# Optimization experiments

Measured on AMD Instinct MI355X. Metric: run time of the kernel, lower is better.

Reference implementation:

```python
import jax, jax.numpy as jnp
import numpy as np

K = 10
ALPHA = 0.1

def setup_inputs() -> dict:
    key = jax.random.key(0)
    k1, k2, k3, k4 = jax.random.split(key, 4)
    N, E, IN, HID, OUT = 100000, 3200000, 512, 256, 64
    x = jax.random.normal(k1, (N, IN), dtype=jnp.float32)
    edge_index = jax.random.randint(k2, (2, E), 0, N, dtype=jnp.int64)
    W1 = jax.random.normal(k3, (IN, HID), dtype=jnp.float32) * (1.0 / np.sqrt(IN))
    b1 = jnp.zeros((HID,), jnp.float32)
    W2 = jax.random.normal(k4, (HID, OUT), dtype=jnp.float32) * (1.0 / np.sqrt(HID))
    b2 = jnp.zeros((OUT,), jnp.float32)
    return {"x": x, "edge_index": edge_index, "W1": W1, "b1": b1, "W2": W2, "b2": b2}

def reference(x, edge_index, W1, b1, W2, b2):
    N = x.shape[0]
    # gcn_norm with self-loops (PyG default for APPNP)
    loop = jnp.arange(N, dtype=edge_index.dtype)
    src = jnp.concatenate([edge_index[0], loop])  # [E+N]
    dst = jnp.concatenate([edge_index[1], loop])
    ones = jnp.ones(src.shape[0], dtype=x.dtype)
    deg = jax.ops.segment_sum(ones, dst, num_segments=N)
    dis = jnp.where(deg > 0, jax.lax.rsqrt(deg), 0.0)
    norm = dis[src] * dis[dst]  # [E+N]

    # 2-layer MLP (dropout disabled: eval mode)
    h = jnp.maximum(x @ W1 + b1, 0.0) @ W2 + b2  # [N, out]

    # K-step PPR diffusion: z <- alpha*h + (1-alpha)*A_hat z
    def step(z, _):
        agg = jax.ops.segment_sum(norm[:, None] * z[src], dst, num_segments=N)
        return ALPHA * h + (1.0 - ALPHA) * agg, None

    z, _ = jax.lax.scan(step, h, None, length=K)
    return jax.nn.log_softmax(z, axis=-1)
```

## Files before the change

### kernel.cpp

```cpp
#include <hip/hip_runtime.h>
#include <hip/hip_bf16.h>

#define ALPHA_F 0.1f
#define KSTEPS 10
#define BKT_SH 9
#define P1_CHUNK 8192

typedef __attribute__((ext_vector_type(8))) short bf16x8;
typedef __attribute__((ext_vector_type(4))) float f32x4;

__device__ __forceinline__ unsigned short f2bf(float f) {
  union { float f; unsigned int u; } v; v.f = f;
  unsigned int u = v.u;
  u += 0x7FFFu + ((u >> 16) & 1u);
  return (unsigned short)(u >> 16);
}
__device__ __forceinline__ float bflo(unsigned int u) { return __uint_as_float(u << 16); }
__device__ __forceinline__ float bfhi(unsigned int u) { return __uint_as_float(u & 0xFFFF0000u); }

__device__ __forceinline__ void gload16(const void* g, void* l) {
  __builtin_amdgcn_global_load_lds(
      (const __attribute__((address_space(1))) void*)g,
      (__attribute__((address_space(3))) void*)l, 16, 0, 0);
}


__global__ __launch_bounds__(256)
void p0_hist(const int* __restrict__ dstv, int E, int* __restrict__ bhist) {
  __shared__ int h[256];
  int t = threadIdx.x;
  h[t] = 0;
  __syncthreads();
  int b0 = blockIdx.x * P1_CHUNK;
  int lim = min(P1_CHUNK, E - b0);
  for (int i = t; i < lim; i += 256) atomicAdd(&h[dstv[b0 + i] >> BKT_SH], 1);
  __syncthreads();
  if (h[t]) atomicAdd(&bhist[t], h[t]);
}

__global__ void p0_scan(const int* __restrict__ bhist, int* __restrict__ bbase,
                        int* __restrict__ gcur, int* __restrict__ rowptr, int N, int E) {
  __shared__ int s[256];
  int t = threadIdx.x;
  int mine = bhist[t];
  s[t] = mine;
  __syncthreads();
  for (int off = 1; off < 256; off <<= 1) {
    int v = (t >= off) ? s[t - off] : 0;
    __syncthreads();
    s[t] += v;
    __syncthreads();
  }
  int excl = s[t] - mine;
  bbase[t] = excl;
  gcur[t] = excl;
  if (t == 0) rowptr[N] = E;
}

__global__ __launch_bounds__(256)
void p1_scatter(const int* __restrict__ srcv, const int* __restrict__ dstv, int E,
                int* __restrict__ gcur, int2* __restrict__ tmp) {
  __shared__ int h[256];
  __shared__ int loc[256];
  int t = threadIdx.x;
  int b0 = blockIdx.x * P1_CHUNK;
  int lim = min(P1_CHUNK, E - b0);
  h[t] = 0;
  __syncthreads();
  for (int i = t; i < lim; i += 256) atomicAdd(&h[dstv[b0 + i] >> BKT_SH], 1);
  __syncthreads();
  loc[t] = h[t] ? atomicAdd(&gcur[t], h[t]) : 0;
  __syncthreads();
  h[t] = 0;
  __syncthreads();
  for (int i = t; i < lim; i += 256) {
    int d = dstv[b0 + i], s = srcv[b0 + i];
    int b = d >> BKT_SH;
    int pos = loc[b] + atomicAdd(&h[b], 1);
    tmp[pos] = make_int2(s, d);
  }
}

__global__ __launch_bounds__(256)
void p2_bucket(const int2* __restrict__ tmp, const int* __restrict__ bbase,
               const int* __restrict__ bhist, int* __restrict__ counts,
               int* __restrict__ rowptr, int2* __restrict__ out, int N) {
  __shared__ int h1[512];
  __shared__ int cur[512];
  __shared__ int s2[256];
  const int t = threadIdx.x;
  const int b = blockIdx.x;
  const int base = bbase[b];
  const int sz = bhist[b];
  const int r0 = b << BKT_SH;
  const int nrows = min(512, N - r0);

  h1[t] = 0; h1[t + 256] = 0;
  __syncthreads();
  for (int i = t; i < sz; i += 256) atomicAdd(&h1[tmp[base + i].y - r0], 1);
  __syncthreads();
  if (t < nrows) counts[r0 + t] = h1[t];
  if (t + 256 < nrows) counts[r0 + t + 256] = h1[t + 256];
  int a = h1[2 * t], c = h1[2 * t + 1];
  s2[t] = a + c;
  __syncthreads();
  for (int off = 1; off < 256; off <<= 1) {
    int v = (t >= off) ? s2[t - off] : 0;
    __syncthreads();
    s2[t] += v;
    __syncthreads();
  }
  int excl2 = s2[t] - (a + c);
  cur[2 * t] = excl2;
  cur[2 * t + 1] = excl2 + a;
  __syncthreads();
  if (t < nrows) rowptr[r0 + t] = base + cur[t];
  if (t + 256 < nrows) rowptr[r0 + t + 256] = base + cur[t + 256];
  __syncthreads();
  for (int i = t; i < sz; i += 256) {
    int2 e = tmp[base + i];
    int p = base + atomicAdd(&cur[e.y - r0], 1);
    out[p] = e;
  }
}

__global__ void k_dis(const int* __restrict__ counts, float* __restrict__ dis, int N) {
  int i = blockIdx.x * 256 + threadIdx.x;
  if (i < N) dis[i] = rsqrtf((float)(counts[i] + 1));
}

__global__ void p3_weights(int2* __restrict__ edges, const float* __restrict__ dis, int E) {
  int i = blockIdx.x * 256 + threadIdx.x;
  if (i >= E) return;
  int2 e = edges[i];
  edges[i] = make_int2(e.x, __float_as_int(dis[e.x] * dis[e.y]));
}


__global__ void k_wconv1(const float* __restrict__ W, unsigned short* __restrict__ WT) {
  int idx = blockIdx.x * 256 + threadIdx.x;
  if (idx >= 512 * 256) return;
  int e = idx & 7, n = (idx >> 3) & 15, q = (idx >> 7) & 7;
  int nsub = (idx >> 10) & 15, kstep = idx >> 14;
  int k = kstep * 64 + q * 8 + e;
  int ncol = nsub * 16 + n;
  WT[idx] = f2bf(W[(size_t)k * 256 + ncol]);
}

__global__ void k_wconv2(const float* __restrict__ W, unsigned short* __restrict__ WT) {
  int idx = blockIdx.x * 256 + threadIdx.x;
  if (idx >= 256 * 64) return;
  int e = idx & 7, n = (idx >> 3) & 15, q = (idx >> 7) & 7;
  int nsub = (idx >> 10) & 3, kstep = idx >> 12;
  int k = kstep * 64 + q * 8 + e;
  int ncol = nsub * 16 + n;
  WT[idx] = f2bf(W[(size_t)k * 64 + ncol]);
}

__global__ __launch_bounds__(512)
void gemm1_kernel(const float* __restrict__ X, const unsigned short* __restrict__ Bt,
                  const float* __restrict__ bias, unsigned short* __restrict__ outT,
                  int M) {
  __shared__ __align__(16) unsigned short Al[8192];
  __shared__ __align__(16) unsigned short Bl[16384];
  const int t = threadIdx.x;
  const int m0 = blockIdx.x * 128;
  const int lane = t & 63;
  const int w = t >> 6;
  const int wm = w >> 2, wn = w & 3;

  const int sm = ((t >> 7) << 4) + (t & 15);
  const int sq = (t >> 4) & 7;
  const int r1 = m0 + sm;
  const int r2 = r1 + 64;
  const bool g1 = r1 < M, g2 = r2 < M;

  f32x4 acc[4][4] = {};

  for (int ks = 0; ks < 8; ++ks) {
    const int kc = ks * 64 + sq * 8;
    uint4 v1 = {0, 0, 0, 0}, v2 = {0, 0, 0, 0};
    if (g1) {
      const float* p = X + (size_t)r1 * 512 + kc;
      float4 a = *(const float4*)p, b = *(const float4*)(p + 4);
      unsigned short* o = (unsigned short*)&v1;
      o[0] = f2bf(a.x); o[1] = f2bf(a.y); o[2] = f2bf(a.z); o[3] = f2bf(a.w);
      o[4] = f2bf(b.x); o[5] = f2bf(b.y); o[6] = f2bf(b.z); o[7] = f2bf(b.w);
    }
    if (g2) {
      const float* p = X + (size_t)r2 * 512 + kc;
      float4 a = *(const float4*)p, b = *(const float4*)(p + 4);
      unsigned short* o = (unsigned short*)&v2;
      o[0] = f2bf(a.x); o[1] = f2bf(a.y); o[2] = f2bf(a.z); o[3] = f2bf(a.w);
      o[4] = f2bf(b.x); o[5] = f2bf(b.y); o[6] = f2bf(b.z); o[7] = f2bf(b.w);
    }
    *(uint4*)&Al[t * 8] = v1;
    *(uint4*)&Al[(t + 512) * 8] = v2;

    const unsigned short* bs = Bt + ks * 16384;
    gload16(bs + (size_t)t * 8,          &Bl[t * 8]);
    gload16(bs + (size_t)(t + 512) * 8,  &Bl[(t + 512) * 8]);
    gload16(bs + (size_t)(t + 1024) * 8, &Bl[(t + 1024) * 8]);
    gload16(bs + (size_t)(t + 1536) * 8, &Bl[(t + 1536) * 8]);
    __syncthreads();

#pragma unroll
    for (int kk = 0; kk < 2; ++kk) {
      bf16x8 af[4], bfv[4];
#pragma unroll
      for (int mi = 0; mi < 4; ++mi)
        af[mi] = *(const bf16x8*)&Al[((wm * 4 + mi) * 128 + kk * 64 + (lane >> 4) * 16 + (lane & 15)) * 8];
#pragma unroll
      for (int ni = 0; ni < 4; ++ni)
        bfv[ni] = *(const bf16x8*)&Bl[((wn * 4 + ni) * 128 + kk * 64 + (lane >> 4) * 16 + (lane & 15)) * 8];
#pragma unroll
      for (int mi = 0; mi < 4; ++mi)
#pragma unroll
        for (int ni = 0; ni < 4; ++ni)
          acc[mi][ni] = __builtin_amdgcn_mfma_f32_16x16x32_bf16(af[mi], bfv[ni], acc[mi][ni], 0, 0, 0);
    }
    __syncthreads();
  }

  unsigned short* ob = outT + (size_t)blockIdx.x * 32768;
#pragma unroll
  for (int mi = 0; mi < 4; ++mi) {
#pragma unroll
    for (int ni = 0; ni < 4; ++ni) {
      int n = wn * 64 + ni * 16 + (lane & 15);
      float bv = bias[n];
      int kstep = n >> 6, q = (n >> 3) & 7, e = n & 7;
#pragma unroll
      for (int j = 0; j < 4; ++j) {
        int lm = wm * 64 + mi * 16 + (lane >> 4) * 4 + j;
        if (m0 + lm < M) {
          float v = fmaxf(acc[mi][ni][j] + bv, 0.f);
          int msub = lm >> 4, mm = lm & 15;
          ob[((((kstep * 8 + msub) * 8 + q) * 16 + mm) * 8) + e] = f2bf(v);
        }
      }
    }
  }
}

__global__ __launch_bounds__(256)
void gemm2_kernel(const unsigned short* __restrict__ At, const unsigned short* __restrict__ Bt,
                  const float* __restrict__ bias, unsigned short* __restrict__ hb, int M) {
  __shared__ __align__(16) unsigned short Al[8192];
  __shared__ __align__(16) unsigned short Bl[4096];
  const int t = threadIdx.x;
  const int m0 = blockIdx.x * 128;
  const int lane = t & 63;
  const int w = t >> 6;
  const int wm = w >> 1, wn = w & 1;

  f32x4 acc[4][2] = {};

  const unsigned short* ab = At + (size_t)blockIdx.x * 32768;
  for (int ks = 0; ks < 4; ++ks) {
    const unsigned short* as = ab + ks * 8192;
    gload16(as + (size_t)t * 8,         &Al[t * 8]);
    gload16(as + (size_t)(t + 256) * 8, &Al[(t + 256) * 8]);
    gload16(as + (size_t)(t + 512) * 8, &Al[(t + 512) * 8]);
    gload16(as + (size_t)(t + 768) * 8, &Al[(t + 768) * 8]);
    const unsigned short* bs = Bt + ks * 4096;
    gload16(bs + (size_t)t * 8,         &Bl[t * 8]);
    gload16(bs + (size_t)(t + 256) * 8, &Bl[(t + 256) * 8]);
    __syncthreads();

#pragma unroll
    for (int kk = 0; kk < 2; ++kk) {
      bf16x8 af[4], bfv[2];
#pragma unroll
      for (int mi = 0; mi < 4; ++mi)
        af[mi] = *(const bf16x8*)&Al[((wm * 4 + mi) * 128 + kk * 64 + (lane >> 4) * 16 + (lane & 15)) * 8];
#pragma unroll
      for (int ni = 0; ni < 2; ++ni)
        bfv[ni] = *(const bf16x8*)&Bl[((wn * 2 + ni) * 128 + kk * 64 + (lane >> 4) * 16 + (lane & 15)) * 8];
#pragma unroll
      for (int mi = 0; mi < 4; ++mi)
#pragma unroll
        for (int ni = 0; ni < 2; ++ni)
          acc[mi][ni] = __builtin_amdgcn_mfma_f32_16x16x32_bf16(af[mi], bfv[ni], acc[mi][ni], 0, 0, 0);
    }
    __syncthreads();
  }

#pragma unroll
  for (int mi = 0; mi < 4; ++mi) {
#pragma unroll
    for (int ni = 0; ni < 2; ++ni) {
      int gn = wn * 32 + ni * 16 + (lane & 15);
      float bv = bias[gn];
#pragma unroll
      for (int j = 0; j < 4; ++j) {
        int gm = m0 + wm * 64 + mi * 16 + (lane >> 4) * 4 + j;
        if (gm < M) hb[(size_t)gm * 64 + gn] = f2bf(acc[mi][ni][j] + bv);
      }
    }
  }
}

template<bool FINAL>
__global__ __launch_bounds__(256)
void prop_kernel(const unsigned short* __restrict__ zin,
                 const unsigned short* __restrict__ hb,
                 void* __restrict__ zout, const int* __restrict__ rowptr,
                 const int2* __restrict__ edges, const float* __restrict__ dis, int N) {
  int wid = (blockIdx.x * 256 + threadIdx.x) >> 6;
  wid = __builtin_amdgcn_readfirstlane(wid);
  if (wid >= N) return;
  const int lane = threadIdx.x & 63;
  const int g  = lane >> 3;
  const int lg = lane & 7;
  const int r = wid;

  float acc[8] = {0.f, 0.f, 0.f, 0.f, 0.f, 0.f, 0.f, 0.f};
  const int start = rowptr[r], end = rowptr[r + 1];
  for (int e = start; e < end; e += 64) {
    int na = end - e; if (na > 64) na = 64;
    int2 ed = make_int2(0, 0);
    if (lane < na) ed = edges[e + lane];
#pragma unroll 4
    for (int j = 0; j < na; j += 8) {
      int jj = j + g;
      int cj = __shfl(ed.x, jj);
      float wj = __shfl(__int_as_float(ed.y), jj);
      uint4 zr = *(const uint4*)(zin + (size_t)cj * 64 + 8 * lg);
      acc[0] += wj * bflo(zr.x); acc[1] += wj * bfhi(zr.x);
      acc[2] += wj * bflo(zr.y); acc[3] += wj * bfhi(zr.y);
      acc[4] += wj * bflo(zr.z); acc[5] += wj * bfhi(zr.z);
      acc[6] += wj * bflo(zr.w); acc[7] += wj * bfhi(zr.w);
    }
  }
#pragma unroll
  for (int k = 0; k < 8; ++k) {
    acc[k] += __shfl_xor(acc[k], 8);
    acc[k] += __shfl_xor(acc[k], 16);
    acc[k] += __shfl_xor(acc[k], 32);
  }

  float dr = dis[r];
  float sw = dr * dr;
  uint4 zs = *(const uint4*)(zin + (size_t)r * 64 + 8 * lg);
  uint4 hr = *(const uint4*)(hb + (size_t)r * 64 + 8 * lg);
  float selfz[8] = { bflo(zs.x), bfhi(zs.x), bflo(zs.y), bfhi(zs.y),
                     bflo(zs.z), bfhi(zs.z), bflo(zs.w), bfhi(zs.w) };
  float hv[8]    = { bflo(hr.x), bfhi(hr.x), bflo(hr.y), bfhi(hr.y),
                     bflo(hr.z), bfhi(hr.z), bflo(hr.w), bfhi(hr.w) };
  float f[8];
#pragma unroll
  for (int k = 0; k < 8; ++k)
    f[k] = ALPHA_F * hv[k] + (1.f - ALPHA_F) * (acc[k] + sw * selfz[k]);

  if (!FINAL) {
    if (g == 0) {
      uint4 o;
      o.x = (unsigned)f2bf(f[0]) | ((unsigned)f2bf(f[1]) << 16);
      o.y = (unsigned)f2bf(f[2]) | ((unsigned)f2bf(f[3]) << 16);
      o.z = (unsigned)f2bf(f[4]) | ((unsigned)f2bf(f[5]) << 16);
      o.w = (unsigned)f2bf(f[6]) | ((unsigned)f2bf(f[7]) << 16);
      *(uint4*)((unsigned short*)zout + (size_t)r * 64 + 8 * lg) = o;
    }
  } else {
    float m = f[0];
#pragma unroll
    for (int k = 1; k < 8; ++k) m = fmaxf(m, f[k]);
    m = fmaxf(m, __shfl_xor(m, 1));
    m = fmaxf(m, __shfl_xor(m, 2));
    m = fmaxf(m, __shfl_xor(m, 4));
    float s = 0.f;
#pragma unroll
    for (int k = 0; k < 8; ++k) s += __expf(f[k] - m);
    s += __shfl_xor(s, 1);
    s += __shfl_xor(s, 2);
    s += __shfl_xor(s, 4);
    float ls = __logf(s);
    if (g == 0) {
      float* op = (float*)zout + (size_t)r * 64 + 8 * lg;
      *(float4*)op       = make_float4(f[0] - m - ls, f[1] - m - ls, f[2] - m - ls, f[3] - m - ls);
      *(float4*)(op + 4) = make_float4(f[4] - m - ls, f[5] - m - ls, f[6] - m - ls, f[7] - m - ls);
    }
  }
}

extern "C" void kernel_launch(void* const* d_in, const int* in_sizes, int n_in,
                              void* d_out, int out_size, void* d_ws, size_t ws_size,
                              hipStream_t stream) {
  const float* x  = (const float*)d_in[0];
  const int*   ei = (const int*)d_in[1];
  const float* W1 = (const float*)d_in[2];
  const float* b1 = (const float*)d_in[3];
  const float* W2 = (const float*)d_in[4];
  const float* b2 = (const float*)d_in[5];

  const int IN = 512, HID = 256, OUT = 64;
  const int N = in_sizes[0] / IN;
  const int E = in_sizes[1] / 2;
  const int* srcv = ei;
  const int* dstv = ei + E;
  const int NBUCK = (N + (1 << BKT_SH) - 1) >> BKT_SH;
  const int MT = (N + 127) / 128;

  char* p = (char*)d_ws;
  auto alloc = [&](size_t bytes) -> void* {
    void* r = (void*)p;
    p += (bytes + 255) & ~(size_t)255;
    return r;
  };
  int*   bhist  = (int*)alloc(256 * 4);
  int*   bbase  = (int*)alloc(256 * 4);
  int*   gcur   = (int*)alloc(256 * 4);
  int*   counts = (int*)alloc((size_t)N * 4);
  float* dis    = (float*)alloc((size_t)N * 4);
  int*   rowptr = (int*)alloc((size_t)(N + 1) * 4);
  int2*  edges  = (int2*)alloc((size_t)E * 8);
  unsigned short* WT1t = (unsigned short*)alloc((size_t)IN * HID * 2);
  unsigned short* WT2t = (unsigned short*)alloc((size_t)HID * OUT * 2);
  unsigned short* hidT = (unsigned short*)alloc((size_t)MT * 32768 * 2);
  unsigned short* hb   = (unsigned short*)alloc((size_t)N * OUT * 2);
  int2* tmp = (int2*)hidT;
  unsigned short* zA = hidT;
  unsigned short* zB = hidT + (size_t)N * OUT;

  hipMemsetAsync(bhist, 0, 256 * 4, stream);

  const int p1blocks = (E + P1_CHUNK - 1) / P1_CHUNK;
  p0_hist<<<p1blocks, 256, 0, stream>>>(dstv, E, bhist);
  p0_scan<<<1, 256, 0, stream>>>(bhist, bbase, gcur, rowptr, N, E);
  p1_scatter<<<p1blocks, 256, 0, stream>>>(srcv, dstv, E, gcur, tmp);
  p2_bucket<<<NBUCK, 256, 0, stream>>>(tmp, bbase, bhist, counts, rowptr, edges, N);
  k_dis<<<(N + 255) / 256, 256, 0, stream>>>(counts, dis, N);
  p3_weights<<<(E + 255) / 256, 256, 0, stream>>>(edges, dis, E);

  k_wconv1<<<(IN * HID + 255) / 256, 256, 0, stream>>>(W1, WT1t);
  k_wconv2<<<(HID * OUT + 255) / 256, 256, 0, stream>>>(W2, WT2t);

  gemm1_kernel<<<MT, 512, 0, stream>>>(x, WT1t, b1, hidT, N);
  gemm2_kernel<<<MT, 256, 0, stream>>>(hidT, WT2t, b2, hb, N);

  const int pblocks = (N + 3) / 4;
  const unsigned short* zcur = hb;
  for (int it = 0; it < KSTEPS - 1; ++it) {
    unsigned short* znext = (it & 1) ? zB : zA;
    prop_kernel<false><<<pblocks, 256, 0, stream>>>(zcur, hb, znext, rowptr, edges, dis, N);
    zcur = znext;
  }
  prop_kernel<true><<<pblocks, 256, 0, stream>>>(zcur, hb, d_out, rowptr, edges, dis, N);
}
```

Measured before the change: 820.2 us.

## Split features into per-XCD quarter planes and fold norm into prescaled features

```diff
diff --git a/kernel.cpp b/kernel.cpp
--- a/kernel.cpp
+++ b/kernel.cpp
@@ -84,7 +84,7 @@
 __global__ __launch_bounds__(256)
 void p2_bucket(const int2* __restrict__ tmp, const int* __restrict__ bbase,
                const int* __restrict__ bhist, int* __restrict__ counts,
-               int* __restrict__ rowptr, int2* __restrict__ out, int N) {
+               int* __restrict__ rowptr, int* __restrict__ col, int N) {
   __shared__ int h1[512];
   __shared__ int cur[512];
   __shared__ int s2[256];
@@ -120,7 +120,7 @@
   for (int i = t; i < sz; i += 256) {
     int2 e = tmp[base + i];
     int p = base + atomicAdd(&cur[e.y - r0], 1);
-    out[p] = e;
+    col[p] = e.x;
   }
 }
 
@@ -129,13 +129,12 @@
   if (i < N) dis[i] = rsqrtf((float)(counts[i] + 1));
 }
 
-__global__ void p3_weights(int2* __restrict__ edges, const float* __restrict__ dis, int E) {
-  int i = blockIdx.x * 256 + threadIdx.x;
-  if (i >= E) return;
-  int2 e = edges[i];
-  edges[i] = make_int2(e.x, __float_as_int(dis[e.x] * dis[e.y]));
-}
-
+__global__ void k_zrow(unsigned short* __restrict__ yA, unsigned short* __restrict__ yB, int N) {
+  int t = threadIdx.x;
+  size_t N1 = (size_t)N + 1;
+  if (t < 64)      yA[((size_t)(t >> 4) * N1 + N) * 16 + (t & 15)] = 0;
+  else { int u = t - 64; yB[((size_t)(u >> 4) * N1 + N) * 16 + (u & 15)] = 0; }
+}
 
 __global__ void k_wconv1(const float* __restrict__ W, unsigned short* __restrict__ WT) {
   int idx = blockIdx.x * 256 + threadIdx.x;
@@ -245,7 +244,8 @@
 
 __global__ __launch_bounds__(256)
 void gemm2_kernel(const unsigned short* __restrict__ At, const unsigned short* __restrict__ Bt,
-                  const float* __restrict__ bias, unsigned short* __restrict__ hb, int M) {
+                  const float* __restrict__ bias, const float* __restrict__ dis,
+                  unsigned short* __restrict__ hq, unsigned short* __restrict__ y0, int M) {
   __shared__ __align__(16) unsigned short Al[8192];
   __shared__ __align__(16) unsigned short Bl[4096];
   const int t = threadIdx.x;
@@ -253,6 +253,7 @@
   const int lane = t & 63;
   const int w = t >> 6;
   const int wm = w >> 1, wn = w & 1;
+  const size_t N1 = (size_t)M + 1;
 
   f32x4 acc[4][2] = {};
 
@@ -292,10 +293,15 @@
     for (int ni = 0; ni < 2; ++ni) {
       int gn = wn * 32 + ni * 16 + (lane & 15);
       float bv = bias[gn];
+      int qq = gn >> 4, cc = gn & 15;
 #pragma unroll
       for (int j = 0; j < 4; ++j) {
         int gm = m0 + wm * 64 + mi * 16 + (lane >> 4) * 4 + j;
-        if (gm < M) hb[(size_t)gm * 64 + gn] = f2bf(acc[mi][ni][j] + bv);
+        if (gm < M) {
+          float v = acc[mi][ni][j] + bv;
+          hq[((size_t)qq * M + gm) * 16 + cc] = f2bf(v);
+          y0[((size_t)qq * N1 + gm) * 16 + cc] = f2bf(dis[gm] * v);
+        }
       }
     }
   }
@@ -303,85 +309,71 @@
 
 template<bool FINAL>
 __global__ __launch_bounds__(256)
-void prop_kernel(const unsigned short* __restrict__ zin,
-                 const unsigned short* __restrict__ hb,
-                 void* __restrict__ zout, const int* __restrict__ rowptr,
-                 const int2* __restrict__ edges, const float* __restrict__ dis, int N) {
-  int wid = (blockIdx.x * 256 + threadIdx.x) >> 6;
-  wid = __builtin_amdgcn_readfirstlane(wid);
-  if (wid >= N) return;
+void prop_q(const unsigned short* __restrict__ yin, const unsigned short* __restrict__ hq,
+            void* __restrict__ yout, const int* __restrict__ rowptr,
+            const int* __restrict__ col, const float* __restrict__ dis, int N, int Q) {
+  const int x = blockIdx.x;
+  const int xcd = x & 7;
+  const int q = xcd >> 1;
+  const int i = (x >> 3) * 2 + (xcd & 1);
+  if (i >= Q) return;
+  int r = i * 4 + (threadIdx.x >> 6);
+  if (r >= N) return;
+  r = __builtin_amdgcn_readfirstlane(r);
   const int lane = threadIdx.x & 63;
-  const int g  = lane >> 3;
-  const int lg = lane & 7;
-  const int r = wid;
-
-  float acc[8] = {0.f, 0.f, 0.f, 0.f, 0.f, 0.f, 0.f, 0.f};
+  const int g = lane >> 3;
+  const int lc = lane & 7;
+  const size_t N1 = (size_t)N + 1;
+  const unsigned short* yq = yin + (size_t)q * N1 * 16;
+
+  float a0 = 0.f, a1 = 0.f;
   const int start = rowptr[r], end = rowptr[r + 1];
   for (int e = start; e < end; e += 64) {
     int na = end - e; if (na > 64) na = 64;
-    int2 ed = make_int2(0, 0);
-    if (lane < na) ed = edges[e + lane];
+    int c = N;
+    if (lane < na) c = col[e + lane];
 #pragma unroll 4
     for (int j = 0; j < na; j += 8) {
-      int jj = j + g;
-      int cj = __shfl(ed.x, jj);
-      float wj = __shfl(__int_as_float(ed.y), jj);
-      uint4 zr = *(const uint4*)(zin + (size_t)cj * 64 + 8 * lg);
-      acc[0] += wj * bflo(zr.x); acc[1] += wj * bfhi(zr.x);
-      acc[2] += wj * bflo(zr.y); acc[3] += wj * bfhi(zr.y);
-      acc[4] += wj * bflo(zr.z); acc[5] += wj * bfhi(zr.z);
-      acc[6] += wj * bflo(zr.w); acc[7] += wj * bfhi(zr.w);
-    }
-  }
-#pragma unroll
-  for (int k = 0; k < 8; ++k) {
-    acc[k] += __shfl_xor(acc[k], 8);
-    acc[k] += __shfl_xor(acc[k], 16);
-    acc[k] += __shfl_xor(acc[k], 32);
-  }
+      int cj = __shfl(c, j + g);
+      unsigned v = *(const unsigned*)(yq + (size_t)cj * 16 + 2 * lc);
+      a0 += bflo(v); a1 += bfhi(v);
+    }
+  }
+  a0 += __shfl_xor(a0, 8);  a1 += __shfl_xor(a1, 8);
+  a0 += __shfl_xor(a0, 16); a1 += __shfl_xor(a1, 16);
+  a0 += __shfl_xor(a0, 32); a1 += __shfl_xor(a1, 32);
 
   float dr = dis[r];
-  float sw = dr * dr;
-  uint4 zs = *(const uint4*)(zin + (size_t)r * 64 + 8 * lg);
-  uint4 hr = *(const uint4*)(hb + (size_t)r * 64 + 8 * lg);
-  float selfz[8] = { bflo(zs.x), bfhi(zs.x), bflo(zs.y), bfhi(zs.y),
-                     bflo(zs.z), bfhi(zs.z), bflo(zs.w), bfhi(zs.w) };
-  float hv[8]    = { bflo(hr.x), bfhi(hr.x), bflo(hr.y), bfhi(hr.y),
-                     bflo(hr.z), bfhi(hr.z), bflo(hr.w), bfhi(hr.w) };
-  float f[8];
-#pragma unroll
-  for (int k = 0; k < 8; ++k)
-    f[k] = ALPHA_F * hv[k] + (1.f - ALPHA_F) * (acc[k] + sw * selfz[k]);
-
+  unsigned sv = *(const unsigned*)(yq + (size_t)r * 16 + 2 * lc);
+  unsigned hv = *(const unsigned*)(hq + ((size_t)q * N + r) * 16 + 2 * lc);
+  float f0 = ALPHA_F * bflo(hv) + (1.f - ALPHA_F) * dr * (a0 + bflo(sv));
+  float f1 = ALPHA_F * bfhi(hv) + (1.f - ALPHA_F) * dr * (a1 + bfhi(sv));
   if (!FINAL) {
     if (g == 0) {
-      uint4 o;
-      o.x = (unsigned)f2bf(f[0]) | ((unsigned)f2bf(f[1]) << 16);
-      o.y = (unsigned)f2bf(f[2]) | ((unsigned)f2bf(f[3]) << 16);
-      o.z = (unsigned)f2bf(f[4]) | ((unsigned)f2bf(f[5]) << 16);
-      o.w = (unsigned)f2bf(f[6]) | ((unsigned)f2bf(f[7]) << 16);
-      *(uint4*)((unsigned short*)zout + (size_t)r * 64 + 8 * lg) = o;
+      unsigned o = (unsigned)f2bf(dr * f0) | ((unsigned)f2bf(dr * f1) << 16);
+      *(unsigned*)((unsigned short*)yout + ((size_t)q * N1 + r) * 16 + 2 * lc) = o;
     }
   } else {
-    float m = f[0];
-#pragma unroll
-    for (int k = 1; k < 8; ++k) m = fmaxf(m, f[k]);
-    m = fmaxf(m, __shfl_xor(m, 1));
-    m = fmaxf(m, __shfl_xor(m, 2));
-    m = fmaxf(m, __shfl_xor(m, 4));
-    float s = 0.f;
-#pragma unroll
-    for (int k = 0; k < 8; ++k) s += __expf(f[k] - m);
-    s += __shfl_xor(s, 1);
-    s += __shfl_xor(s, 2);
-    s += __shfl_xor(s, 4);
-    float ls = __logf(s);
     if (g == 0) {
-      float* op = (float*)zout + (size_t)r * 64 + 8 * lg;
-      *(float4*)op       = make_float4(f[0] - m - ls, f[1] - m - ls, f[2] - m - ls, f[3] - m - ls);
-      *(float4*)(op + 4) = make_float4(f[4] - m - ls, f[5] - m - ls, f[6] - m - ls, f[7] - m - ls);
-    }
-  }
+      *(float2*)((float*)yout + ((size_t)q * N + r) * 16 + 2 * lc) = make_float2(f0, f1);
+    }
+  }
+}
+
+__global__ __launch_bounds__(256)
+void k_lsm(const float* __restrict__ zfin, float* __restrict__ out, int N) {
+  int r = (blockIdx.x * 256 + threadIdx.x) >> 6;
+  if (r >= N) return;
+  int lane = threadIdx.x & 63;
+  float v = zfin[((size_t)(lane >> 4) * N + r) * 16 + (lane & 15)];
+  float m = v;
+#pragma unroll
+  for (int off = 32; off; off >>= 1) m = fmaxf(m, __shfl_xor(m, off));
+  float e = __expf(v - m);
+  float s = e;
+#pragma unroll
+  for (int off = 32; off; off >>= 1) s += __shfl_xor(s, off);
+  out[(size_t)r * 64 + lane] = v - m - __logf(s);
 }
 
 extern "C" void kernel_launch(void* const* d_in, const int* in_sizes, int n_in,
@@ -401,6 +393,7 @@
   const int* dstv = ei + E;
   const int NBUCK = (N + (1 << BKT_SH) - 1) >> BKT_SH;
   const int MT = (N + 127) / 128;
+  const size_t N1 = (size_t)N + 1;
 
   char* p = (char*)d_ws;
   auto alloc = [&](size_t bytes) -> void* {
@@ -414,14 +407,22 @@
   int*   counts = (int*)alloc((size_t)N * 4);
   float* dis    = (float*)alloc((size_t)N * 4);
   int*   rowptr = (int*)alloc((size_t)(N + 1) * 4);
-  int2*  edges  = (int2*)alloc((size_t)E * 8);
+  int*   col    = (int*)alloc((size_t)E * 4);
   unsigned short* WT1t = (unsigned short*)alloc((size_t)IN * HID * 2);
   unsigned short* WT2t = (unsigned short*)alloc((size_t)HID * OUT * 2);
-  unsigned short* hidT = (unsigned short*)alloc((size_t)MT * 32768 * 2);
-  unsigned short* hb   = (unsigned short*)alloc((size_t)N * OUT * 2);
-  int2* tmp = (int2*)hidT;
-  unsigned short* zA = hidT;
-  unsigned short* zB = hidT + (size_t)N * OUT;
+  unsigned short* hq   = (unsigned short*)alloc((size_t)N * 64 * 2);
+  unsigned short* yA   = (unsigned short*)alloc(N1 * 64 * 2);
+  size_t hidT_bytes = (size_t)MT * 32768 * 2;
+  size_t zfin_bytes = (size_t)N * 64 * 4;
+  size_t yB_bytes   = N1 * 64 * 2;
+  size_t R_bytes = hidT_bytes;
+  if ((size_t)E * 8 > R_bytes) R_bytes = (size_t)E * 8;
+  if (zfin_bytes + 256 + yB_bytes > R_bytes) R_bytes = zfin_bytes + 256 + yB_bytes;
+  char* R = (char*)alloc(R_bytes);
+  int2* tmp = (int2*)R;
+  unsigned short* hidT = (unsigned short*)R;
+  float* zfin = (float*)R;
+  unsigned short* yB = (unsigned short*)(R + ((zfin_bytes + 255) & ~(size_t)255));
 
   hipMemsetAsync(bhist, 0, 256 * 4, stream);
 
@@ -429,22 +430,24 @@
   p0_hist<<<p1blocks, 256, 0, stream>>>(dstv, E, bhist);
   p0_scan<<<1, 256, 0, stream>>>(bhist, bbase, gcur, rowptr, N, E);
   p1_scatter<<<p1blocks, 256, 0, stream>>>(srcv, dstv, E, gcur, tmp);
-  p2_bucket<<<NBUCK, 256, 0, stream>>>(tmp, bbase, bhist, counts, rowptr, edges, N);
+  p2_bucket<<<NBUCK, 256, 0, stream>>>(tmp, bbase, bhist, counts, rowptr, col, N);
   k_dis<<<(N + 255) / 256, 256, 0, stream>>>(counts, dis, N);
-  p3_weights<<<(E + 255) / 256, 256, 0, stream>>>(edges, dis, E);
 
   k_wconv1<<<(IN * HID + 255) / 256, 256, 0, stream>>>(W1, WT1t);
   k_wconv2<<<(HID * OUT + 255) / 256, 256, 0, stream>>>(W2, WT2t);
 
   gemm1_kernel<<<MT, 512, 0, stream>>>(x, WT1t, b1, hidT, N);
-  gemm2_kernel<<<MT, 256, 0, stream>>>(hidT, WT2t, b2, hb, N);
-
-  const int pblocks = (N + 3) / 4;
-  const unsigned short* zcur = hb;
+  gemm2_kernel<<<MT, 256, 0, stream>>>(hidT, WT2t, b2, dis, hq, yA, N);
+  k_zrow<<<1, 128, 0, stream>>>(yA, yB, N);
+
+  const int Q = (N + 3) / 4;
+  const int pblocks = 8 * ((Q + 1) / 2);
+  const unsigned short* ycur = yA;
   for (int it = 0; it < KSTEPS - 1; ++it) {
-    unsigned short* znext = (it & 1) ? zB : zA;
-    prop_kernel<false><<<pblocks, 256, 0, stream>>>(zcur, hb, znext, rowptr, edges, dis, N);
-    zcur = znext;
-  }
-  prop_kernel<true><<<pblocks, 256, 0, stream>>>(zcur, hb, d_out, rowptr, edges, dis, N);
-}
+    unsigned short* ynext = (it & 1) ? yA : yB;
+    prop_q<false><<<pblocks, 256, 0, stream>>>(ycur, hq, ynext, rowptr, col, dis, N, Q);
+    ycur = ynext;
+  }
+  prop_q<true><<<pblocks, 256, 0, stream>>>(ycur, hq, zfin, rowptr, col, dis, N, Q);
+  k_lsm<<<(N + 3) / 4, 256, 0, stream>>>(zfin, (float*)d_out, N);
+}
```

Result: slower. 1.571 ms (+91.6%).

## Prescale features by inverse-sqrt degree and use padded index-only CSR

Applied to the files above, without the earlier changes.

```diff
diff --git a/kernel.cpp b/kernel.cpp
--- a/kernel.cpp
+++ b/kernel.cpp
@@ -5,6 +5,7 @@
 #define KSTEPS 10
 #define BKT_SH 9
 #define P1_CHUNK 8192
+#define MAXPAD_PER_BUCKET (512 * 32)
 
 typedef __attribute__((ext_vector_type(8))) short bf16x8;
 typedef __attribute__((ext_vector_type(4))) float f32x4;
@@ -39,7 +40,7 @@
 }
 
 __global__ void p0_scan(const int* __restrict__ bhist, int* __restrict__ bbase,
-                        int* __restrict__ gcur, int* __restrict__ rowptr, int N, int E) {
+                        int* __restrict__ gcur) {
   __shared__ int s[256];
   int t = threadIdx.x;
   int mine = bhist[t];
@@ -54,7 +55,6 @@
   int excl = s[t] - mine;
   bbase[t] = excl;
   gcur[t] = excl;
-  if (t == 0) rowptr[N] = E;
 }
 
 __global__ __launch_bounds__(256)
@@ -84,13 +84,14 @@
 __global__ __launch_bounds__(256)
 void p2_bucket(const int2* __restrict__ tmp, const int* __restrict__ bbase,
                const int* __restrict__ bhist, int* __restrict__ counts,
-               int* __restrict__ rowptr, int2* __restrict__ out, int N) {
+               int* __restrict__ rowptr, int* __restrict__ col, int N) {
   __shared__ int h1[512];
   __shared__ int cur[512];
   __shared__ int s2[256];
   const int t = threadIdx.x;
   const int b = blockIdx.x;
   const int base = bbase[b];
+  const int pbase = base + b * MAXPAD_PER_BUCKET;
   const int sz = bhist[b];
   const int r0 = b << BKT_SH;
   const int nrows = min(512, N - r0);
@@ -99,9 +100,8 @@
   __syncthreads();
   for (int i = t; i < sz; i += 256) atomicAdd(&h1[tmp[base + i].y - r0], 1);
   __syncthreads();
-  if (t < nrows) counts[r0 + t] = h1[t];
-  if (t + 256 < nrows) counts[r0 + t + 256] = h1[t + 256];
-  int a = h1[2 * t], c = h1[2 * t + 1];
+  int a = (h1[2 * t] + 31) & ~31;
+  int c = (h1[2 * t + 1] + 31) & ~31;
   s2[t] = a + c;
   __syncthreads();
   for (int off = 1; off < 256; off <<= 1) {
@@ -114,13 +114,20 @@
   cur[2 * t] = excl2;
   cur[2 * t + 1] = excl2 + a;
   __syncthreads();
-  if (t < nrows) rowptr[r0 + t] = base + cur[t];
-  if (t + 256 < nrows) rowptr[r0 + t + 256] = base + cur[t + 256];
+  if (t < nrows)       { rowptr[r0 + t] = pbase + cur[t];             counts[r0 + t] = h1[t]; }
+  if (t + 256 < nrows) { rowptr[r0 + t + 256] = pbase + cur[t + 256]; counts[r0 + t + 256] = h1[t + 256]; }
   __syncthreads();
   for (int i = t; i < sz; i += 256) {
     int2 e = tmp[base + i];
-    int p = base + atomicAdd(&cur[e.y - r0], 1);
-    out[p] = e;
+    int p = pbase + atomicAdd(&cur[e.y - r0], 1);
+    col[p] = e.x;
+  }
+  __syncthreads();
+  for (int i = t; i < nrows; i += 256) {
+    int cnt = h1[i];
+    int c32 = (cnt + 31) & ~31;
+    int ps = pbase + cur[i];
+    for (int k = cnt; k < c32; ++k) col[ps++] = N;
   }
 }
 
@@ -129,13 +136,11 @@
   if (i < N) dis[i] = rsqrtf((float)(counts[i] + 1));
 }
 
-__global__ void p3_weights(int2* __restrict__ edges, const float* __restrict__ dis, int E) {
-  int i = blockIdx.x * 256 + threadIdx.x;
-  if (i >= E) return;
-  int2 e = edges[i];
-  edges[i] = make_int2(e.x, __float_as_int(dis[e.x] * dis[e.y]));
-}
-
+__global__ void k_zrow(unsigned short* __restrict__ yA, unsigned short* __restrict__ yB, int N) {
+  int t = threadIdx.x;
+  if (t < 64) yA[(size_t)N * 64 + t] = 0;
+  else        yB[(size_t)N * 64 + (t - 64)] = 0;
+}
 
 __global__ void k_wconv1(const float* __restrict__ W, unsigned short* __restrict__ WT) {
   int idx = blockIdx.x * 256 + threadIdx.x;
@@ -245,7 +250,8 @@
 
 __global__ __launch_bounds__(256)
 void gemm2_kernel(const unsigned short* __restrict__ At, const unsigned short* __restrict__ Bt,
-                  const float* __restrict__ bias, unsigned short* __restrict__ hb, int M) {
+                  const float* __restrict__ bias, const float* __restrict__ dis,
+                  unsigned short* __restrict__ hb, unsigned short* __restrict__ y0, int M) {
   __shared__ __align__(16) unsigned short Al[8192];
   __shared__ __align__(16) unsigned short Bl[4096];
   const int t = threadIdx.x;
@@ -295,7 +301,11 @@
 #pragma unroll
       for (int j = 0; j < 4; ++j) {
         int gm = m0 + wm * 64 + mi * 16 + (lane >> 4) * 4 + j;
-        if (gm < M) hb[(size_t)gm * 64 + gn] = f2bf(acc[mi][ni][j] + bv);
+        if (gm < M) {
+          float v = acc[mi][ni][j] + bv;
+          hb[(size_t)gm * 64 + gn] = f2bf(v);
+          y0[(size_t)gm * 64 + gn] = f2bf(dis[gm] * v);
+        }
       }
     }
   }
@@ -303,35 +313,42 @@
 
 template<bool FINAL>
 __global__ __launch_bounds__(256)
-void prop_kernel(const unsigned short* __restrict__ zin,
+void prop_kernel(const unsigned short* __restrict__ yin,
                  const unsigned short* __restrict__ hb,
-                 void* __restrict__ zout, const int* __restrict__ rowptr,
-                 const int2* __restrict__ edges, const float* __restrict__ dis, int N) {
+                 void* __restrict__ yout,
+                 const int* __restrict__ rowptr, const int* __restrict__ counts,
+                 const int* __restrict__ col, const float* __restrict__ dis, int N) {
   int wid = (blockIdx.x * 256 + threadIdx.x) >> 6;
   wid = __builtin_amdgcn_readfirstlane(wid);
   if (wid >= N) return;
   const int lane = threadIdx.x & 63;
-  const int g  = lane >> 3;
+  const int g = lane >> 3;
   const int lg = lane & 7;
   const int r = wid;
 
+  const int start = rowptr[r];
+  const int cnt = counts[r];
+  const int iters = (cnt + 31) >> 5;
+  const float dr = dis[r];
+  uint4 zs = *(const uint4*)(yin + (size_t)r * 64 + 8 * lg);
+  uint4 hr = *(const uint4*)(hb + (size_t)r * 64 + 8 * lg);
+
   float acc[8] = {0.f, 0.f, 0.f, 0.f, 0.f, 0.f, 0.f, 0.f};
-  const int start = rowptr[r], end = rowptr[r + 1];
-  for (int e = start; e < end; e += 64) {
-    int na = end - e; if (na > 64) na = 64;
-    int2 ed = make_int2(0, 0);
-    if (lane < na) ed = edges[e + lane];
-#pragma unroll 4
-    for (int j = 0; j < na; j += 8) {
-      int jj = j + g;
-      int cj = __shfl(ed.x, jj);
-      float wj = __shfl(__int_as_float(ed.y), jj);
-      uint4 zr = *(const uint4*)(zin + (size_t)cj * 64 + 8 * lg);
-      acc[0] += wj * bflo(zr.x); acc[1] += wj * bfhi(zr.x);
-      acc[2] += wj * bflo(zr.y); acc[3] += wj * bfhi(zr.y);
-      acc[4] += wj * bflo(zr.z); acc[5] += wj * bfhi(zr.z);
-      acc[6] += wj * bflo(zr.w); acc[7] += wj * bfhi(zr.w);
-    }
+  const int* cp = col + start + 4 * g;
+  for (int it = 0; it < iters; ++it, cp += 32) {
+    int4 cc = *(const int4*)cp;
+    uint4 z0 = *(const uint4*)(yin + (size_t)cc.x * 64 + 8 * lg);
+    uint4 z1 = *(const uint4*)(yin + (size_t)cc.y * 64 + 8 * lg);
+    uint4 z2 = *(const uint4*)(yin + (size_t)cc.z * 64 + 8 * lg);
+    uint4 z3 = *(const uint4*)(yin + (size_t)cc.w * 64 + 8 * lg);
+    acc[0] += bflo(z0.x); acc[1] += bfhi(z0.x); acc[2] += bflo(z0.y); acc[3] += bfhi(z0.y);
+    acc[4] += bflo(z0.z); acc[5] += bfhi(z0.z); acc[6] += bflo(z0.w); acc[7] += bfhi(z0.w);
+    acc[0] += bflo(z1.x); acc[1] += bfhi(z1.x); acc[2] += bflo(z1.y); acc[3] += bfhi(z1.y);
+    acc[4] += bflo(z1.z); acc[5] += bfhi(z1.z); acc[6] += bflo(z1.w); acc[7] += bfhi(z1.w);
+    acc[0] += bflo(z2.x); acc[1] += bfhi(z2.x); acc[2] += bflo(z2.y); acc[3] += bfhi(z2.y);
+    acc[4] += bflo(z2.z); acc[5] += bfhi(z2.z); acc[6] += bflo(z2.w); acc[7] += bfhi(z2.w);
+    acc[0] += bflo(z3.x); acc[1] += bfhi(z3.x); acc[2] += bflo(z3.y); acc[3] += bfhi(z3.y);
+    acc[4] += bflo(z3.z); acc[5] += bfhi(z3.z); acc[6] += bflo(z3.w); acc[7] += bfhi(z3.w);
   }
 #pragma unroll
   for (int k = 0; k < 8; ++k) {
@@ -340,10 +357,6 @@
     acc[k] += __shfl_xor(acc[k], 32);
   }
 
-  float dr = dis[r];
-  float sw = dr * dr;
-  uint4 zs = *(const uint4*)(zin + (size_t)r * 64 + 8 * lg);
-  uint4 hr = *(const uint4*)(hb + (size_t)r * 64 + 8 * lg);
   float selfz[8] = { bflo(zs.x), bfhi(zs.x), bflo(zs.y), bfhi(zs.y),
                      bflo(zs.z), bfhi(zs.z), bflo(zs.w), bfhi(zs.w) };
   float hv[8]    = { bflo(hr.x), bfhi(hr.x), bflo(hr.y), bfhi(hr.y),
@@ -351,16 +364,16 @@
   float f[8];
 #pragma unroll
   for (int k = 0; k < 8; ++k)
-    f[k] = ALPHA_F * hv[k] + (1.f - ALPHA_F) * (acc[k] + sw * selfz[k]);
+    f[k] = ALPHA_F * hv[k] + (1.f - ALPHA_F) * dr * (acc[k] + selfz[k]);
 
   if (!FINAL) {
     if (g == 0) {
       uint4 o;
-      o.x = (unsigned)f2bf(f[0]) | ((unsigned)f2bf(f[1]) << 16);
-      o.y = (unsigned)f2bf(f[2]) | ((unsigned)f2bf(f[3]) << 16);
-      o.z = (unsigned)f2bf(f[4]) | ((unsigned)f2bf(f[5]) << 16);
-      o.w = (unsigned)f2bf(f[6]) | ((unsigned)f2bf(f[7]) << 16);
-      *(uint4*)((unsigned short*)zout + (size_t)r * 64 + 8 * lg) = o;
+      o.x = (unsigned)f2bf(dr * f[0]) | ((unsigned)f2bf(dr * f[1]) << 16);
+      o.y = (unsigned)f2bf(dr * f[2]) | ((unsigned)f2bf(dr * f[3]) << 16);
+      o.z = (unsigned)f2bf(dr * f[4]) | ((unsigned)f2bf(dr * f[5]) << 16);
+      o.w = (unsigned)f2bf(dr * f[6]) | ((unsigned)f2bf(dr * f[7]) << 16);
+      *(uint4*)((unsigned short*)yout + (size_t)r * 64 + 8 * lg) = o;
     }
   } else {
     float m = f[0];
@@ -377,7 +390,7 @@
     s += __shfl_xor(s, 4);
     float ls = __logf(s);
     if (g == 0) {
-      float* op = (float*)zout + (size_t)r * 64 + 8 * lg;
+      float* op = (float*)yout + (size_t)r * 64 + 8 * lg;
       *(float4*)op       = make_float4(f[0] - m - ls, f[1] - m - ls, f[2] - m - ls, f[3] - m - ls);
       *(float4*)(op + 4) = make_float4(f[4] - m - ls, f[5] - m - ls, f[6] - m - ls, f[7] - m - ls);
     }
@@ -401,6 +414,7 @@
   const int* dstv = ei + E;
   const int NBUCK = (N + (1 << BKT_SH) - 1) >> BKT_SH;
   const int MT = (N + 127) / 128;
+  const size_t N1 = (size_t)N + 1;
 
   char* p = (char*)d_ws;
   auto alloc = [&](size_t bytes) -> void* {
@@ -414,37 +428,42 @@
   int*   counts = (int*)alloc((size_t)N * 4);
   float* dis    = (float*)alloc((size_t)N * 4);
   int*   rowptr = (int*)alloc((size_t)(N + 1) * 4);
-  int2*  edges  = (int2*)alloc((size_t)E * 8);
+  int*   col    = (int*)alloc(((size_t)E + 256 * MAXPAD_PER_BUCKET) * 4);
   unsigned short* WT1t = (unsigned short*)alloc((size_t)IN * HID * 2);
   unsigned short* WT2t = (unsigned short*)alloc((size_t)HID * OUT * 2);
-  unsigned short* hidT = (unsigned short*)alloc((size_t)MT * 32768 * 2);
   unsigned short* hb   = (unsigned short*)alloc((size_t)N * OUT * 2);
-  int2* tmp = (int2*)hidT;
-  unsigned short* zA = hidT;
-  unsigned short* zB = hidT + (size_t)N * OUT;
+  unsigned short* yA   = (unsigned short*)alloc(N1 * OUT * 2);
+  size_t hidT_bytes = (size_t)MT * 32768 * 2;
+  size_t R_bytes = hidT_bytes;
+  if ((size_t)E * 8 > R_bytes) R_bytes = (size_t)E * 8;
+  if (N1 * OUT * 2 > R_bytes) R_bytes = N1 * OUT * 2;
+  char* R = (char*)alloc(R_bytes);
+  int2* tmp = (int2*)R;
+  unsigned short* hidT = (unsigned short*)R;
+  unsigned short* yB = (unsigned short*)R;
 
   hipMemsetAsync(bhist, 0, 256 * 4, stream);
 
   const int p1blocks = (E + P1_CHUNK - 1) / P1_CHUNK;
   p0_hist<<<p1blocks, 256, 0, stream>>>(dstv, E, bhist);
-  p0_scan<<<1, 256, 0, stream>>>(bhist, bbase, gcur, rowptr, N, E);
+  p0_scan<<<1, 256, 0, stream>>>(bhist, bbase, gcur);
   p1_scatter<<<p1blocks, 256, 0, stream>>>(srcv, dstv, E, gcur, tmp);
-  p2_bucket<<<NBUCK, 256, 0, stream>>>(tmp, bbase, bhist, counts, rowptr, edges, N);
+  p2_bucket<<<NBUCK, 256, 0, stream>>>(tmp, bbase, bhist, counts, rowptr, col, N);
   k_dis<<<(N + 255) / 256, 256, 0, stream>>>(counts, dis, N);
-  p3_weights<<<(E + 255) / 256, 256, 0, stream>>>(edges, dis, E);
 
   k_wconv1<<<(IN * HID + 255) / 256, 256, 0, stream>>>(W1, WT1t);
   k_wconv2<<<(HID * OUT + 255) / 256, 256, 0, stream>>>(W2, WT2t);
 
   gemm1_kernel<<<MT, 512, 0, stream>>>(x, WT1t, b1, hidT, N);
-  gemm2_kernel<<<MT, 256, 0, stream>>>(hidT, WT2t, b2, hb, N);
+  gemm2_kernel<<<MT, 256, 0, stream>>>(hidT, WT2t, b2, dis, hb, yA, N);
+  k_zrow<<<1, 128, 0, stream>>>(yA, yB, N);
 
   const int pblocks = (N + 3) / 4;
-  const unsigned short* zcur = hb;
+  const unsigned short* ycur = yA;
   for (int it = 0; it < KSTEPS - 1; ++it) {
-    unsigned short* znext = (it & 1) ? zB : zA;
-    prop_kernel<false><<<pblocks, 256, 0, stream>>>(zcur, hb, znext, rowptr, edges, dis, N);
-    zcur = znext;
-  }
-  prop_kernel<true><<<pblocks, 256, 0, stream>>>(zcur, hb, d_out, rowptr, edges, dis, N);
-}
+    unsigned short* ynext = (it & 1) ? yA : yB;
+    prop_kernel<false><<<pblocks, 256, 0, stream>>>(ycur, hb, ynext, rowptr, counts, col, dis, N);
+    ycur = ynext;
+  }
+  prop_kernel<true><<<pblocks, 256, 0, stream>>>(ycur, hb, d_out, rowptr, counts, col, dis, N);
+}
```

After: 764.8 us. -6.8%, faster.
